# Kernel tuning notes

Measured on AMD Instinct MI355X. Metric: run time of the kernel, lower is better.

Reference implementation:

```python
import jax, jax.numpy as jnp
import numpy as np

EPS = 1e-5

def _bn(x, g, b, m, v):
    # inference-mode BatchNorm2d over NCHW
    inv = g / jnp.sqrt(v + EPS)
    return x * inv[None, :, None, None] + (b - m * inv)[None, :, None, None]

def _adder2d(x, w, stride, pad):
    # AdderNet 'convolution': out = -sum_{c,kh,kw} |patch - w|
    B, C, H, W = x.shape
    O, _, k, _ = w.shape
    xp = jnp.pad(x, ((0, 0), (0, 0), (pad, pad), (pad, pad)))
    Ho = (H + 2 * pad - k) // stride + 1
    Wo = (W + 2 * pad - k) // stride + 1
    # unfold: [B, C, k*k, Ho, Wo] with (C, kh, kw) ordering matching w.reshape
    cols = jnp.stack([xp[:, :, i:i + stride * Ho:stride, j:j + stride * Wo:stride]
                      for i in range(k) for j in range(k)], axis=2)
    cols = cols.reshape(B, C * k * k, Ho * Wo)            # [B, CKK, L]
    wf = w.reshape(O, C * k * k)                          # [O, CKK]
    out = -jnp.sum(jnp.abs(cols[:, None, :, :] - wf[None, :, :, None]), axis=2)  # [B,O,L]
    return out.reshape(B, O, Ho, Wo)

def setup_inputs() -> dict:
    key = jax.random.key(0)
    ks = jax.random.split(key, 16)
    C = 64
    return {
        "x": jax.random.normal(ks[0], (4, C, 32, 32), jnp.float32),
        "bn1_g": jax.random.uniform(ks[1], (C,), jnp.float32),
        "bn1_b": jax.random.normal(ks[2], (C,), jnp.float32),
        "bn1_m": jax.random.normal(ks[3], (C,), jnp.float32),
        "bn1_v": jax.random.uniform(ks[4], (C,), jnp.float32),
        "w1": jax.random.normal(ks[5], (C, C, 3, 3), jnp.float32),
        "bn2_g": jax.random.uniform(ks[6], (C,), jnp.float32),
        "bn2_b": jax.random.normal(ks[7], (C,), jnp.float32),
        "bn2_m": jax.random.normal(ks[8], (C,), jnp.float32),
        "bn2_v": jax.random.uniform(ks[9], (C,), jnp.float32),
        "w2": jax.random.normal(ks[10], (C, C, 3, 3), jnp.float32),
        "fc1_w": jax.random.normal(ks[11], (C // 16, C), jnp.float32) * 0.1,
        "fc1_b": jax.random.normal(ks[12], (C // 16,), jnp.float32) * 0.1,
        "fc2_w": jax.random.normal(ks[13], (C, C // 16), jnp.float32) * 0.1,
        "fc2_b": jax.random.normal(ks[14], (C,), jnp.float32) * 0.1,
    }

def reference(x, bn1_g, bn1_b, bn1_m, bn1_v, w1,
              bn2_g, bn2_b, bn2_m, bn2_v, w2,
              fc1_w, fc1_b, fc2_w, fc2_b):
    out = jax.nn.relu(_bn(x, bn1_g, bn1_b, bn1_m, bn1_v))
    shortcut = x  # stride==1 and in_planes==planes -> identity shortcut
    out = _adder2d(out, w1, 1, 1)
    out = _adder2d(jax.nn.relu(_bn(out, bn2_g, bn2_b, bn2_m, bn2_v)), w2, 1, 1)
    # SE gate: global avg pool -> fc1 -> relu -> fc2 -> sigmoid
    s = out.mean(axis=(2, 3))                              # [B, planes]
    h = jax.nn.relu(s @ fc1_w.T + fc1_b)
    g = jax.nn.sigmoid(h @ fc2_w.T + fc2_b)
    return out * g[:, :, None, None] + shortcut
```

## Files before the change

kernel.cpp:

```cpp
#include <hip/hip_runtime.h>
#include <math.h>

#define NELEM   262144
#define NW      36864
#define EPS_BN  1e-5f
#define QSCALE  65536.0f
#define QBIAS_F (16.0f * 65536.0f + 0.5f)
#define QB_U    1048576u
#define QINV    (1.0f / 65536.0f)

__device__ __forceinline__ unsigned sad_acc(unsigned a, unsigned b, unsigned acc) {
    asm("v_sad_u32 %0, %1, %2, %0" : "+v"(acc) : "v"(a), "v"(b));
    return acc;
}

__global__ __launch_bounds__(256) void prep_kernel(
    const float* __restrict__ x,
    const float* __restrict__ g1, const float* __restrict__ b1,
    const float* __restrict__ m1, const float* __restrict__ v1,
    const float* __restrict__ w1,
    const float* __restrict__ g2, const float* __restrict__ b2,
    const float* __restrict__ m2, const float* __restrict__ v2,
    const float* __restrict__ w2,
    unsigned* __restrict__ qx, unsigned* __restrict__ qw1,
    unsigned* __restrict__ qw2, float* __restrict__ bn2c)
{
    int i = blockIdx.x * 256 + threadIdx.x;
    if (i < NELEM) {
        int c = (i >> 10) & 63;
        float inv = g1[c] * rsqrtf(v1[c] + EPS_BN);
        float bet = b1[c] - m1[c] * inv;
        float a = fmaxf(fmaf(x[i], inv, bet), 0.f);
        qx[i] = (unsigned)fmaf(a, QSCALE, QBIAS_F);
    }
    int j = i - NELEM;
    if (j >= 0 && j < NW) qw1[j] = (unsigned)fmaf(w1[j], QSCALE, QBIAS_F);
    int k = j - NW;
    if (k >= 0 && k < NW) qw2[k] = (unsigned)fmaf(w2[k], QSCALE, QBIAS_F);
    int l = k - NW;
    if (l >= 0 && l < 64) {
        float inv = g2[l] * rsqrtf(v2[l] + EPS_BN);
        bn2c[l]      = -inv * QINV;
        bn2c[l + 64] = b2[l] - m2[l] * inv;
    }
}

template<int MODE>
__global__ __launch_bounds__(256, 4) void adder_kernel(
    const unsigned* __restrict__ qsrc, const unsigned* __restrict__ qw,
    const float* __restrict__ bn2c,
    unsigned* __restrict__ qout, float* __restrict__ fout,
    float* __restrict__ sbuf)
{
    __shared__ union {
        unsigned tile[32][6][36];
        unsigned red[16][16][16];
    } sh;
    __shared__ unsigned wlds[2][64][12];

    const int blk = blockIdx.x;
    const int sp  = blk & 7;
    const int og  = (blk >> 3) & 31;
    const int b   = blk >> 8;
    const int t   = threadIdx.x;
    const int pos = t & 15;
    const int cq  = t >> 4;
    const int y_i = pos >> 2;
    const int x0  = (pos & 3) * 8;

    for (int i = t; i < 1152; i += 256) {
        int o_i = i / 576;
        int rem = i - o_i * 576;
        int c   = rem / 9;
        int kk  = rem - c * 9;
        wlds[o_i][c][kk] = qw[(og * 2 + o_i) * 576 + c * 9 + kk];
    }

    unsigned acc[2][8];
#pragma unroll
    for (int oo = 0; oo < 2; ++oo)
#pragma unroll
        for (int xi = 0; xi < 8; ++xi) acc[oo][xi] = 0u;

    for (int ch0 = 0; ch0 < 64; ch0 += 32) {
        __syncthreads();
#pragma unroll
        for (int kk = 0; kk < 6; ++kk) {
            int i   = t + kk * 256;
            int cc  = i / 48;
            int rem = i - cc * 48;
            int yy  = rem >> 3;
            int gx  = (rem & 7) * 4;
            int gy  = sp * 4 - 1 + yy;
            uint4 v = make_uint4(QB_U, QB_U, QB_U, QB_U);
            if (gy >= 0 && gy < 32)
                v = *reinterpret_cast<const uint4*>(
                    qsrc + (((b * 64 + ch0 + cc) * 32 + gy) * 32 + gx));
            unsigned* dst = &sh.tile[cc][yy][1 + gx];
            dst[0] = v.x; dst[1] = v.y; dst[2] = v.z; dst[3] = v.w;
        }
        for (int i = t; i < 384; i += 256) {
            int cc  = i / 12;
            int rem = i - cc * 12;
            int yy  = rem >> 1;
            sh.tile[cc][yy][(rem & 1) ? 33 : 0] = QB_U;
        }
        __syncthreads();

#pragma unroll
        for (int j = 0; j < 2; ++j) {
            const int cl = cq * 2 + j;
            const int c  = ch0 + cl;
            unsigned p[3][12];
#pragma unroll
            for (int r = 0; r < 3; ++r) {
                uint4 a0 = *reinterpret_cast<const uint4*>(&sh.tile[cl][y_i + r][x0]);
                uint4 a1 = *reinterpret_cast<const uint4*>(&sh.tile[cl][y_i + r][x0 + 4]);
                uint4 a2 = *reinterpret_cast<const uint4*>(&sh.tile[cl][y_i + r][x0 + 8]);
                p[r][0] = a0.x; p[r][1]  = a0.y; p[r][2]  = a0.z; p[r][3]  = a0.w;
                p[r][4] = a1.x; p[r][5]  = a1.y; p[r][6]  = a1.z; p[r][7]  = a1.w;
                p[r][8] = a2.x; p[r][9]  = a2.y; p[r][10] = a2.z; p[r][11] = a2.w;
            }
#pragma unroll
            for (int oo = 0; oo < 2; ++oo) {
                uint4 wa = *reinterpret_cast<const uint4*>(&wlds[oo][c][0]);
                uint4 wb = *reinterpret_cast<const uint4*>(&wlds[oo][c][4]);
                unsigned w8 = wlds[oo][c][8];
                unsigned wv[9] = {wa.x, wa.y, wa.z, wa.w,
                                  wb.x, wb.y, wb.z, wb.w, w8};
#pragma unroll
                for (int kh = 0; kh < 3; ++kh)
#pragma unroll
                    for (int kw = 0; kw < 3; ++kw) {
                        unsigned ww = wv[kh * 3 + kw];
#pragma unroll
                        for (int xi = 0; xi < 8; ++xi)
                            acc[oo][xi] = sad_acc(p[kh][xi + kw], ww, acc[oo][xi]);
                    }
            }
        }
    }

    __syncthreads();
    {
        unsigned* dst = &sh.red[cq][pos][0];
        *reinterpret_cast<uint4*>(dst + 0)  = make_uint4(acc[0][0], acc[0][1], acc[0][2], acc[0][3]);
        *reinterpret_cast<uint4*>(dst + 4)  = make_uint4(acc[0][4], acc[0][5], acc[0][6], acc[0][7]);
        *reinterpret_cast<uint4*>(dst + 8)  = make_uint4(acc[1][0], acc[1][1], acc[1][2], acc[1][3]);
        *reinterpret_cast<uint4*>(dst + 12) = make_uint4(acc[1][4], acc[1][5], acc[1][6], acc[1][7]);
    }
    __syncthreads();

    const int oo2 = t >> 7;
    const int s   = t & 127;
    const int yy2 = s >> 5;
    const int xx2 = s & 31;
    const int pp  = yy2 * 4 + (xx2 >> 3);
    const int z   = (oo2 << 3) | (xx2 & 7);
    unsigned total = 0;
#pragma unroll
    for (int q = 0; q < 16; ++q) total += sh.red[q][pp][z];

    const int o   = og * 2 + oo2;
    const int idx = ((b * 64 + o) * 32 + sp * 4 + yy2) * 32 + xx2;
    const float accf = (float)total;

    if (MODE == 0) {
        float a2 = fmaxf(fmaf(accf, bn2c[o], bn2c[o + 64]), 0.f);
        qout[idx] = (unsigned)fmaf(a2, QSCALE, QBIAS_F);
    } else {
        float v = -accf * QINV;
        fout[idx] = v;
        float sum = v;
#pragma unroll
        for (int off = 32; off > 0; off >>= 1)
            sum += __shfl_down(sum, off, 64);
        if ((t & 63) == 0) atomicAdd(&sbuf[b * 64 + o], sum);
    }
}

__global__ __launch_bounds__(256) void gate_kernel(
    const float* __restrict__ out2, const float* __restrict__ x,
    const float* __restrict__ sbuf,
    const float* __restrict__ fc1w, const float* __restrict__ fc1b,
    const float* __restrict__ fc2w, const float* __restrict__ fc2b,
    float* __restrict__ out)
{
    const int bo = blockIdx.x;
    const int b  = bo >> 6;
    const int o  = bo & 63;
    const int t  = threadIdx.x;

    __shared__ float ss[64];
    if (t < 64) ss[t] = sbuf[b * 64 + t] * (1.f / 1024.f);
    __syncthreads();

    float h[4];
#pragma unroll
    for (int j = 0; j < 4; ++j) {
        float a = fc1b[j];
#pragma unroll
        for (int c = 0; c < 64; ++c) a += ss[c] * fc1w[j * 64 + c];
        h[j] = fmaxf(a, 0.f);
    }
    float zz = fc2b[o];
#pragma unroll
    for (int j = 0; j < 4; ++j) zz += h[j] * fc2w[o * 4 + j];
    float g = 1.f / (1.f + __expf(-zz));

    const int base = bo * 1024 + t * 4;
    float4 v  = *reinterpret_cast<const float4*>(out2 + base);
    float4 xv = *reinterpret_cast<const float4*>(x + base);
    float4 r;
    r.x = v.x * g + xv.x;
    r.y = v.y * g + xv.y;
    r.z = v.z * g + xv.z;
    r.w = v.w * g + xv.w;
    *reinterpret_cast<float4*>(out + base) = r;
}

extern "C" void kernel_launch(void* const* d_in, const int* in_sizes, int n_in,
                              void* d_out, int out_size, void* d_ws, size_t ws_size,
                              hipStream_t stream)
{
    const float* x    = (const float*)d_in[0];
    const float* bn1g = (const float*)d_in[1];
    const float* bn1b = (const float*)d_in[2];
    const float* bn1m = (const float*)d_in[3];
    const float* bn1v = (const float*)d_in[4];
    const float* w1   = (const float*)d_in[5];
    const float* bn2g = (const float*)d_in[6];
    const float* bn2b = (const float*)d_in[7];
    const float* bn2m = (const float*)d_in[8];
    const float* bn2v = (const float*)d_in[9];
    const float* w2   = (const float*)d_in[10];
    const float* fc1w = (const float*)d_in[11];
    const float* fc1b = (const float*)d_in[12];
    const float* fc2w = (const float*)d_in[13];
    const float* fc2b = (const float*)d_in[14];

    unsigned* ws    = (unsigned*)d_ws;
    unsigned* qx    = ws;
    unsigned* qout1 = ws + NELEM;
    float*    out2  = (float*)(ws + 2 * NELEM);
    unsigned* qw1   = ws + 3 * NELEM;
    unsigned* qw2   = ws + 3 * NELEM + NW;
    float*    bn2c  = (float*)(ws + 3 * NELEM + 2 * NW);
    float*    sbuf  = (float*)(ws + 3 * NELEM + 2 * NW + 128);

    hipMemsetAsync(sbuf, 0, 256 * sizeof(float), stream);
    prep_kernel<<<1313, 256, 0, stream>>>(x, bn1g, bn1b, bn1m, bn1v, w1,
                                          bn2g, bn2b, bn2m, bn2v, w2,
                                          qx, qw1, qw2, bn2c);
    adder_kernel<0><<<1024, 256, 0, stream>>>(qx,    qw1, bn2c, qout1, nullptr, nullptr);
    adder_kernel<1><<<1024, 256, 0, stream>>>(qout1, qw2, nullptr, nullptr, out2, sbuf);
    gate_kernel<<<256, 256, 0, stream>>>(out2, x, sbuf, fc1w, fc1b, fc2w, fc2b,
                                         (float*)d_out);
}
```

Baseline: 132.0 us.

## Store padded quantized activations in global memory and read patches directly

Activations are now written into pre-padded 34x36 per-channel images so the adder kernels load their 3x3 patch rows straight from global memory (through cache) instead of staging a tile in LDS with two barriers per channel chunk. The prep kernel writes the padded input, sets the border of the intermediate buffer, and zeroes the SE sum buffer, which removes the separate memset. This drops the LDS tile and its synchronisation. In exchange each thread issues more global loads for overlapping rows and relies on L1/L2 reuse.

```diff
diff --git a/kernel.cpp b/kernel.cpp
--- a/kernel.cpp
+++ b/kernel.cpp
@@ -3,6 +3,9 @@
 
 #define NELEM   262144
 #define NW      36864
+#define PIMG    1296
+#define PADN    331776
+#define NBORD   295936
 #define EPS_BN  1e-5f
 #define QSCALE  65536.0f
 #define QBIAS_F (16.0f * 65536.0f + 0.5f)
@@ -22,27 +25,49 @@
     const float* __restrict__ g2, const float* __restrict__ b2,
     const float* __restrict__ m2, const float* __restrict__ v2,
     const float* __restrict__ w2,
-    unsigned* __restrict__ qx, unsigned* __restrict__ qw1,
-    unsigned* __restrict__ qw2, float* __restrict__ bn2c)
+    unsigned* __restrict__ qxp, unsigned* __restrict__ qout1p,
+    unsigned* __restrict__ qw1, unsigned* __restrict__ qw2,
+    float* __restrict__ bn2c, float* __restrict__ sbuf)
 {
     int i = blockIdx.x * 256 + threadIdx.x;
-    if (i < NELEM) {
-        int c = (i >> 10) & 63;
-        float inv = g1[c] * rsqrtf(v1[c] + EPS_BN);
-        float bet = b1[c] - m1[c] * inv;
-        float a = fmaxf(fmaf(x[i], inv, bet), 0.f);
-        qx[i] = (unsigned)fmaf(a, QSCALE, QBIAS_F);
-    }
-    int j = i - NELEM;
-    if (j >= 0 && j < NW) qw1[j] = (unsigned)fmaf(w1[j], QSCALE, QBIAS_F);
-    int k = j - NW;
-    if (k >= 0 && k < NW) qw2[k] = (unsigned)fmaf(w2[k], QSCALE, QBIAS_F);
+    if (i < NBORD) {
+        int bc  = i / 1156;
+        int rc  = i - bc * 1156;
+        int r   = rc / 34;
+        int col = rc - r * 34;
+        unsigned q = QB_U;
+        if (r > 0 && r < 33 && col > 0 && col < 33) {
+            int c = bc & 63;
+            float inv = g1[c] * rsqrtf(v1[c] + EPS_BN);
+            float bet = b1[c] - m1[c] * inv;
+            float a = fmaxf(fmaf(x[(bc * 32 + (r - 1)) * 32 + (col - 1)], inv, bet), 0.f);
+            q = (unsigned)fmaf(a, QSCALE, QBIAS_F);
+        }
+        qxp[bc * PIMG + r * 36 + col] = q;
+        return;
+    }
+    int j = i - NBORD;
+    if (j < NBORD) {
+        int bc  = j / 1156;
+        int rc  = j - bc * 1156;
+        int r   = rc / 34;
+        int col = rc - r * 34;
+        if (r == 0 || r == 33 || col == 0 || col == 33)
+            qout1p[bc * PIMG + r * 36 + col] = QB_U;
+        return;
+    }
+    int k = j - NBORD;
+    if (k < NW) { qw1[k] = (unsigned)fmaf(w1[k], QSCALE, QBIAS_F); return; }
     int l = k - NW;
-    if (l >= 0 && l < 64) {
-        float inv = g2[l] * rsqrtf(v2[l] + EPS_BN);
-        bn2c[l]      = -inv * QINV;
-        bn2c[l + 64] = b2[l] - m2[l] * inv;
-    }
+    if (l < NW) { qw2[l] = (unsigned)fmaf(w2[l], QSCALE, QBIAS_F); return; }
+    int m = l - NW;
+    if (m < 64) {
+        float inv = g2[m] * rsqrtf(v2[m] + EPS_BN);
+        bn2c[m]      = -inv * QINV;
+        bn2c[m + 64] = b2[m] - m2[m] * inv;
+    }
+    int s = m - 64;
+    if (s >= 0 && s < 256) sbuf[s] = 0.f;
 }
 
 template<int MODE>
@@ -52,11 +77,8 @@
     unsigned* __restrict__ qout, float* __restrict__ fout,
     float* __restrict__ sbuf)
 {
-    __shared__ union {
-        unsigned tile[32][6][36];
-        unsigned red[16][16][16];
-    } sh;
     __shared__ unsigned wlds[2][64][12];
+    __shared__ unsigned red[16][16][16];
 
     const int blk = blockIdx.x;
     const int sp  = blk & 7;
@@ -75,6 +97,7 @@
         int kk  = rem - c * 9;
         wlds[o_i][c][kk] = qw[(og * 2 + o_i) * 576 + c * 9 + kk];
     }
+    __syncthreads();
 
     unsigned acc[2][8];
 #pragma unroll
@@ -82,68 +105,43 @@
 #pragma unroll
         for (int xi = 0; xi < 8; ++xi) acc[oo][xi] = 0u;
 
-    for (int ch0 = 0; ch0 < 64; ch0 += 32) {
-        __syncthreads();
-#pragma unroll
-        for (int kk = 0; kk < 6; ++kk) {
-            int i   = t + kk * 256;
-            int cc  = i / 48;
-            int rem = i - cc * 48;
-            int yy  = rem >> 3;
-            int gx  = (rem & 7) * 4;
-            int gy  = sp * 4 - 1 + yy;
-            uint4 v = make_uint4(QB_U, QB_U, QB_U, QB_U);
-            if (gy >= 0 && gy < 32)
-                v = *reinterpret_cast<const uint4*>(
-                    qsrc + (((b * 64 + ch0 + cc) * 32 + gy) * 32 + gx));
-            unsigned* dst = &sh.tile[cc][yy][1 + gx];
-            dst[0] = v.x; dst[1] = v.y; dst[2] = v.z; dst[3] = v.w;
+    const unsigned* base = qsrc + (size_t)(b * 64 + cq * 4) * PIMG
+                                + (sp * 4 + y_i) * 36 + x0;
+#pragma unroll
+    for (int j = 0; j < 4; ++j) {
+        const unsigned* pc = base + j * PIMG;
+        unsigned p[3][12];
+#pragma unroll
+        for (int r = 0; r < 3; ++r) {
+            uint4 a0 = *reinterpret_cast<const uint4*>(pc + r * 36);
+            uint4 a1 = *reinterpret_cast<const uint4*>(pc + r * 36 + 4);
+            uint4 a2 = *reinterpret_cast<const uint4*>(pc + r * 36 + 8);
+            p[r][0] = a0.x; p[r][1]  = a0.y; p[r][2]  = a0.z; p[r][3]  = a0.w;
+            p[r][4] = a1.x; p[r][5]  = a1.y; p[r][6]  = a1.z; p[r][7]  = a1.w;
+            p[r][8] = a2.x; p[r][9]  = a2.y; p[r][10] = a2.z; p[r][11] = a2.w;
         }
-        for (int i = t; i < 384; i += 256) {
-            int cc  = i / 12;
-            int rem = i - cc * 12;
-            int yy  = rem >> 1;
-            sh.tile[cc][yy][(rem & 1) ? 33 : 0] = QB_U;
+        const int c = cq * 4 + j;
+#pragma unroll
+        for (int oo = 0; oo < 2; ++oo) {
+            uint4 wa = *reinterpret_cast<const uint4*>(&wlds[oo][c][0]);
+            uint4 wb = *reinterpret_cast<const uint4*>(&wlds[oo][c][4]);
+            unsigned w8 = wlds[oo][c][8];
+            unsigned wv[9] = {wa.x, wa.y, wa.z, wa.w,
+                              wb.x, wb.y, wb.z, wb.w, w8};
+#pragma unroll
+            for (int kh = 0; kh < 3; ++kh)
+#pragma unroll
+                for (int kw = 0; kw < 3; ++kw) {
+                    unsigned ww = wv[kh * 3 + kw];
+#pragma unroll
+                    for (int xi = 0; xi < 8; ++xi)
+                        acc[oo][xi] = sad_acc(p[kh][xi + kw], ww, acc[oo][xi]);
+                }
         }
-        __syncthreads();
-
-#pragma unroll
-        for (int j = 0; j < 2; ++j) {
-            const int cl = cq * 2 + j;
-            const int c  = ch0 + cl;
-            unsigned p[3][12];
-#pragma unroll
-            for (int r = 0; r < 3; ++r) {
-                uint4 a0 = *reinterpret_cast<const uint4*>(&sh.tile[cl][y_i + r][x0]);
-                uint4 a1 = *reinterpret_cast<const uint4*>(&sh.tile[cl][y_i + r][x0 + 4]);
-                uint4 a2 = *reinterpret_cast<const uint4*>(&sh.tile[cl][y_i + r][x0 + 8]);
-                p[r][0] = a0.x; p[r][1]  = a0.y; p[r][2]  = a0.z; p[r][3]  = a0.w;
-                p[r][4] = a1.x; p[r][5]  = a1.y; p[r][6]  = a1.z; p[r][7]  = a1.w;
-                p[r][8] = a2.x; p[r][9]  = a2.y; p[r][10] = a2.z; p[r][11] = a2.w;
-            }
-#pragma unroll
-            for (int oo = 0; oo < 2; ++oo) {
-                uint4 wa = *reinterpret_cast<const uint4*>(&wlds[oo][c][0]);
-                uint4 wb = *reinterpret_cast<const uint4*>(&wlds[oo][c][4]);
-                unsigned w8 = wlds[oo][c][8];
-                unsigned wv[9] = {wa.x, wa.y, wa.z, wa.w,
-                                  wb.x, wb.y, wb.z, wb.w, w8};
-#pragma unroll
-                for (int kh = 0; kh < 3; ++kh)
-#pragma unroll
-                    for (int kw = 0; kw < 3; ++kw) {
-                        unsigned ww = wv[kh * 3 + kw];
-#pragma unroll
-                        for (int xi = 0; xi < 8; ++xi)
-                            acc[oo][xi] = sad_acc(p[kh][xi + kw], ww, acc[oo][xi]);
-                    }
-            }
-        }
-    }
-
-    __syncthreads();
+    }
+
     {
-        unsigned* dst = &sh.red[cq][pos][0];
+        unsigned* dst = &red[cq][pos][0];
         *reinterpret_cast<uint4*>(dst + 0)  = make_uint4(acc[0][0], acc[0][1], acc[0][2], acc[0][3]);
         *reinterpret_cast<uint4*>(dst + 4)  = make_uint4(acc[0][4], acc[0][5], acc[0][6], acc[0][7]);
         *reinterpret_cast<uint4*>(dst + 8)  = make_uint4(acc[1][0], acc[1][1], acc[1][2], acc[1][3]);
@@ -159,18 +157,19 @@
     const int z   = (oo2 << 3) | (xx2 & 7);
     unsigned total = 0;
 #pragma unroll
-    for (int q = 0; q < 16; ++q) total += sh.red[q][pp][z];
-
-    const int o   = og * 2 + oo2;
-    const int idx = ((b * 64 + o) * 32 + sp * 4 + yy2) * 32 + xx2;
+    for (int q = 0; q < 16; ++q) total += red[q][pp][z];
+
+    const int o    = og * 2 + oo2;
+    const int gy   = sp * 4 + yy2;
     const float accf = (float)total;
 
     if (MODE == 0) {
         float a2 = fmaxf(fmaf(accf, bn2c[o], bn2c[o + 64]), 0.f);
-        qout[idx] = (unsigned)fmaf(a2, QSCALE, QBIAS_F);
+        qout[(size_t)(b * 64 + o) * PIMG + (gy + 1) * 36 + (xx2 + 1)] =
+            (unsigned)fmaf(a2, QSCALE, QBIAS_F);
     } else {
         float v = -accf * QINV;
-        fout[idx] = v;
+        fout[((b * 64 + o) * 32 + gy) * 32 + xx2] = v;
         float sum = v;
 #pragma unroll
         for (int off = 32; off > 0; off >>= 1)
@@ -239,21 +238,20 @@
     const float* fc2w = (const float*)d_in[13];
     const float* fc2b = (const float*)d_in[14];
 
-    unsigned* ws    = (unsigned*)d_ws;
-    unsigned* qx    = ws;
-    unsigned* qout1 = ws + NELEM;
-    float*    out2  = (float*)(ws + 2 * NELEM);
-    unsigned* qw1   = ws + 3 * NELEM;
-    unsigned* qw2   = ws + 3 * NELEM + NW;
-    float*    bn2c  = (float*)(ws + 3 * NELEM + 2 * NW);
-    float*    sbuf  = (float*)(ws + 3 * NELEM + 2 * NW + 128);
-
-    hipMemsetAsync(sbuf, 0, 256 * sizeof(float), stream);
-    prep_kernel<<<1313, 256, 0, stream>>>(x, bn1g, bn1b, bn1m, bn1v, w1,
+    unsigned* ws     = (unsigned*)d_ws;
+    unsigned* qxp    = ws;
+    unsigned* qout1p = ws + PADN;
+    float*    out2   = (float*)(ws + 2 * PADN);
+    unsigned* qw1    = ws + 2 * PADN + NELEM;
+    unsigned* qw2    = ws + 2 * PADN + NELEM + NW;
+    float*    bn2c   = (float*)(ws + 2 * PADN + NELEM + 2 * NW);
+    float*    sbuf   = (float*)(ws + 2 * PADN + NELEM + 2 * NW + 128);
+
+    prep_kernel<<<2602, 256, 0, stream>>>(x, bn1g, bn1b, bn1m, bn1v, w1,
                                           bn2g, bn2b, bn2m, bn2v, w2,
-                                          qx, qw1, qw2, bn2c);
-    adder_kernel<0><<<1024, 256, 0, stream>>>(qx,    qw1, bn2c, qout1, nullptr, nullptr);
-    adder_kernel<1><<<1024, 256, 0, stream>>>(qout1, qw2, nullptr, nullptr, out2, sbuf);
+                                          qxp, qout1p, qw1, qw2, bn2c, sbuf);
+    adder_kernel<0><<<1024, 256, 0, stream>>>(qxp,    qw1, bn2c, qout1p, nullptr, nullptr);
+    adder_kernel<1><<<1024, 256, 0, stream>>>(qout1p, qw2, nullptr, nullptr, out2, sbuf);
     gate_kernel<<<256, 256, 0, stream>>>(out2, x, sbuf, fc1w, fc1b, fc2w, fc2b,
                                          (float*)d_out);
 }
```

Result: faster. 114.7 us (-13.1%).
